# Performance work log

Hardware: AMD Instinct MI355X
Metric: run time of the kernel (lower is better)

## Reference

```python
import jax, jax.numpy as jnp
import numpy as np

R = 8      # num_dilation_rates
B = 32
C_IN = 21
C = 128    # C_out
L = 4096
K = 2      # kernel_size


def _causal_conv(x, w, dilation, pad, length):
    # x: [B, C, L], w: [Co, Ci, K]. Left-pad by `pad`, dilated valid conv, keep first L.
    # Matches Causal_conv1d: type 'A' -> pad=K(=2); type 'B' -> pad=dilation*(K-1)+1.
    y = jax.lax.conv_general_dilated(
        x, w, window_strides=(1,), padding=[(pad, 0)],
        rhs_dilation=(dilation,), dimension_numbers=('NCH', 'OIH', 'NCH'))
    return y[:, :, :length]


def setup_inputs() -> dict:
    key = jax.random.key(0)
    ks = jax.random.split(key, 10)
    s = 0.1  # small init scale (stands in for xavier)
    return {
        'x': jax.random.normal(ks[0], (B, C_IN, L), jnp.float32),
        'z': jax.random.normal(ks[1], (B, 1, L), jnp.float32),
        'w0': jax.random.normal(ks[2], (C, C_IN), jnp.float32) * s,          # causal_blocks[0] 1x1 conv
        'b0': jnp.zeros((C,), jnp.float32),
        'signal_w': jax.random.normal(ks[3], (R, C, C, K), jnp.float32) * s,  # dilated kernel-2 convs
        'gate_w': jax.random.normal(ks[4], (R, C, C, K), jnp.float32) * s,
        'cond_signal_w': jax.random.normal(ks[5], (R, C), jnp.float32) * s,   # Conv1d(1, C, 1) weights
        'cond_gate_w': jax.random.normal(ks[6], (R, C), jnp.float32) * s,
        'res_w': jax.random.normal(ks[7], (R, C, C), jnp.float32) * s,        # 1x1 residual convs
        'skip_w': jax.random.normal(ks[8], (R, C, C), jnp.float32) * s,       # 1x1 skip convs
    }


def reference(x, z, w0, b0, signal_w, gate_w, cond_signal_w, cond_gate_w, res_w, skip_w):
    length = x.shape[2]
    # initial 1x1 conv with bias
    h = jnp.einsum('oi,bil->bol', w0, x) + b0[None, :, None]
    orig = h
    cum_skip = jnp.zeros_like(h)
    zf = z[:, 0, :]  # [B, L]
    n_rates = signal_w.shape[0]
    for ii in range(n_rates):
        d = 2 ** ii
        pad = K if ii == 0 else d * (K - 1) + 1  # mask 'A' for layer 0, 'B' otherwise
        signal = _causal_conv(h, signal_w[ii], d, pad, length) \
            + jnp.einsum('o,bl->bol', cond_signal_w[ii], zf)
        gate = _causal_conv(h, gate_w[ii], d, pad, length) \
            + jnp.einsum('o,bl->bol', cond_gate_w[ii], zf)
        g = signal * jax.nn.sigmoid(gate)                      # gated activation
        skip = jnp.einsum('oi,bil->bol', skip_w[ii], g)
        res = jnp.einsum('oi,bil->bol', res_w[ii], g)
        h = (orig + res) if ii == 0 else (res + g)             # matches torch control flow
        cum_skip = cum_skip + skip
    return h, cum_skip
```

## Files before the change

### kernel.cpp

```cpp
#include <hip/hip_runtime.h>
#include <hip/hip_bf16.h>

#define RR 8
#define BB 32
#define CIN 21
#define CC 128
#define LL 4096
#define TT 64
#define SROW 132
#define GP 136
#define PADT 132
#define LP (LL + PADT)

typedef short s16x8 __attribute__((ext_vector_type(8)));
typedef float f32x4 __attribute__((ext_vector_type(4)));

__device__ __forceinline__ unsigned short f2b(float f) {
    __hip_bfloat16 h = __float2bfloat16(f);
    return *reinterpret_cast<unsigned short*>(&h);
}
__device__ __forceinline__ float b2f(unsigned short u) {
    __hip_bfloat16 h;
    *reinterpret_cast<unsigned short*>(&h) = u;
    return __bfloat162float(h);
}
__device__ __forceinline__ unsigned int packsplit(float v) {
    unsigned short hi = f2b(v);
    unsigned short lo = f2b(v - b2f(hi));
    return ((unsigned int)hi << 16) | (unsigned int)lo;
}
__device__ __forceinline__ float unpacksum(unsigned int u) {
    return b2f((unsigned short)(u >> 16)) + b2f((unsigned short)(u & 0xffffu));
}

__device__ __forceinline__ void unpack8(const unsigned int* p, s16x8& hi, s16x8& lo) {
    uint4 u0 = *reinterpret_cast<const uint4*>(p);
    uint4 u1 = *reinterpret_cast<const uint4*>(p + 4);
    union { int i[4]; s16x8 v; } H, L;
    H.i[0] = __builtin_amdgcn_perm(u0.y, u0.x, 0x07060302u);
    L.i[0] = __builtin_amdgcn_perm(u0.y, u0.x, 0x05040100u);
    H.i[1] = __builtin_amdgcn_perm(u0.w, u0.z, 0x07060302u);
    L.i[1] = __builtin_amdgcn_perm(u0.w, u0.z, 0x05040100u);
    H.i[2] = __builtin_amdgcn_perm(u1.y, u1.x, 0x07060302u);
    L.i[2] = __builtin_amdgcn_perm(u1.y, u1.x, 0x05040100u);
    H.i[3] = __builtin_amdgcn_perm(u1.w, u1.z, 0x07060302u);
    L.i[3] = __builtin_amdgcn_perm(u1.w, u1.z, 0x05040100u);
    hi = H.v; lo = L.v;
}

__global__ void prep_kernel(const float* __restrict__ sw, const float* __restrict__ gw,
                            const float* __restrict__ skw, const float* __restrict__ rew,
                            unsigned short* __restrict__ WsgH, unsigned short* __restrict__ WsgL,
                            unsigned short* __restrict__ WkrH, unsigned short* __restrict__ WkrL) {
    int idx = blockIdx.x * 256 + threadIdx.x;
    int r = idx >> 16;
    int rem = idx & 65535;
    int o = rem >> 8;
    int k = rem & 255;
    int c = k & 127;
    int tap = k >> 7;
    float v = (o < 128) ? sw[(((r * 128 + o) * 128 + c) << 1) + tap]
                        : gw[(((r * 128 + (o - 128)) * 128 + c) << 1) + tap];
    unsigned short hi = f2b(v);
    WsgH[idx] = hi;
    WsgL[idx] = f2b(v - b2f(hi));
    if (idx < RR * 256 * 128) {
        int r2 = idx >> 15;
        int rem2 = idx & 32767;
        int o2 = rem2 >> 7;
        int c2 = rem2 & 127;
        float v2 = (o2 < 128) ? skw[(r2 * 128 + o2) * 128 + c2]
                              : rew[(r2 * 128 + (o2 - 128)) * 128 + c2];
        unsigned short hi2 = f2b(v2);
        WkrH[idx] = hi2;
        WkrL[idx] = f2b(v2 - b2f(hi2));
    }
}

__global__ void zero_pad_kernel(unsigned int* __restrict__ hA, unsigned int* __restrict__ hB) {
    int idx = blockIdx.x * 256 + threadIdx.x;
    int c = idx & 127;
    int r = (idx >> 7) % PADT;
    int b = idx / (PADT * 128);
    size_t off = ((size_t)b * LP + r) * CC + c;
    hA[off] = 0u;
    hB[off] = 0u;
}

__global__ void proj_kernel(const float* __restrict__ x, const float* __restrict__ w0,
                            const float* __restrict__ b0, unsigned int* __restrict__ h0) {
    int idx = blockIdx.x * 256 + threadIdx.x;
    int c = idx & 127;
    int t = (idx >> 7) & (LL - 1);
    int b = idx >> 19;
    const float* xb = x + (size_t)b * CIN * LL + t;
    const float* w = w0 + c * CIN;
    float acc = b0[c];
#pragma unroll
    for (int i = 0; i < CIN; i++) acc = fmaf(w[i], xb[i * LL], acc);
    h0[((size_t)b * LP + PADT + t) * CC + c] = packsplit(acc);
}

__global__ void __launch_bounds__(512, 4) layer_kernel(
    const unsigned int* __restrict__ hcur,
    unsigned int* __restrict__ hnext,
    float* __restrict__ skipbuf,
    const unsigned short* __restrict__ WsgH, const unsigned short* __restrict__ WsgL,
    const unsigned short* __restrict__ WkrH, const unsigned short* __restrict__ WkrL,
    const float* __restrict__ csw, const float* __restrict__ cgw,
    const float* __restrict__ z,
    float* __restrict__ out,
    int off0, int first, int last) {
    __shared__ unsigned int sBuf[2 * TT * GP / 2];
    unsigned short* sGhi = (unsigned short*)sBuf;
    unsigned short* sGlo = sGhi + TT * GP;

    int tid = threadIdx.x;
    int b = blockIdx.x >> 6;
    int t0 = (blockIdx.x & 63) * TT;

    int wave = tid >> 6;
    int lane = tid & 63;
    int l15 = lane & 15;
    int quad = lane >> 4;

    const unsigned int* hb = hcur + (size_t)b * LP * CC;

    uint4 stg[4];
    {
        const unsigned int* src0 = hb + (size_t)(PADT + t0 - off0) * CC;
#pragma unroll
        for (int j = 0; j < 4; j++) {
            int flat = tid + 512 * j;
            int row = flat >> 5;
            int c16 = flat & 31;
            uint4 v = *(const uint4*)(src0 + (size_t)row * CC + c16 * 4);
            *(uint4*)(sBuf + row * SROW + c16 * 4) = v;
        }
        const unsigned int* src1 = hb + (size_t)(PADT + t0 - 1) * CC;
#pragma unroll
        for (int j = 0; j < 4; j++) {
            int flat = tid + 512 * j;
            int row = flat >> 5;
            int c16 = flat & 31;
            stg[j] = *(const uint4*)(src1 + (size_t)row * CC + c16 * 4);
        }
    }
    __syncthreads();

    f32x4 acc1[4][2];
#pragma unroll
    for (int m = 0; m < 4; m++)
#pragma unroll
        for (int n = 0; n < 2; n++) acc1[m][n] = (f32x4){0.f, 0.f, 0.f, 0.f};

#pragma unroll
    for (int kk = 0; kk < 4; kk++) {
        const int cb = kk * 32 + quad * 8;
        s16x8 Ah[4], Al[4];
#pragma unroll
        for (int m = 0; m < 4; m++)
            unpack8(sBuf + (m * 16 + l15) * SROW + cb, Ah[m], Al[m]);
#pragma unroll
        for (int n = 0; n < 2; n++) {
            int o = (wave + 8 * n) * 16 + l15;
            s16x8 Bh = *(const s16x8*)(WsgH + o * 256 + kk * 32 + quad * 8);
            s16x8 Bl = *(const s16x8*)(WsgL + o * 256 + kk * 32 + quad * 8);
#pragma unroll
            for (int m = 0; m < 4; m++) {
                acc1[m][n] = __builtin_amdgcn_mfma_f32_16x16x32_bf16(Ah[m], Bh, acc1[m][n], 0, 0, 0);
                acc1[m][n] = __builtin_amdgcn_mfma_f32_16x16x32_bf16(Al[m], Bh, acc1[m][n], 0, 0, 0);
                acc1[m][n] = __builtin_amdgcn_mfma_f32_16x16x32_bf16(Ah[m], Bl, acc1[m][n], 0, 0, 0);
            }
        }
    }
    __syncthreads();

#pragma unroll
    for (int j = 0; j < 4; j++) {
        int flat = tid + 512 * j;
        int row = flat >> 5;
        int c16 = flat & 31;
        *(uint4*)(sBuf + row * SROW + c16 * 4) = stg[j];
    }
    __syncthreads();

#pragma unroll
    for (int kk = 0; kk < 4; kk++) {
        const int cb = kk * 32 + quad * 8;
        s16x8 Ah[4], Al[4];
#pragma unroll
        for (int m = 0; m < 4; m++)
            unpack8(sBuf + (m * 16 + l15) * SROW + cb, Ah[m], Al[m]);
#pragma unroll
        for (int n = 0; n < 2; n++) {
            int o = (wave + 8 * n) * 16 + l15;
            s16x8 Bh = *(const s16x8*)(WsgH + o * 256 + (kk + 4) * 32 + quad * 8);
            s16x8 Bl = *(const s16x8*)(WsgL + o * 256 + (kk + 4) * 32 + quad * 8);
#pragma unroll
            for (int m = 0; m < 4; m++) {
                acc1[m][n] = __builtin_amdgcn_mfma_f32_16x16x32_bf16(Ah[m], Bh, acc1[m][n], 0, 0, 0);
                acc1[m][n] = __builtin_amdgcn_mfma_f32_16x16x32_bf16(Al[m], Bh, acc1[m][n], 0, 0, 0);
                acc1[m][n] = __builtin_amdgcn_mfma_f32_16x16x32_bf16(Ah[m], Bl, acc1[m][n], 0, 0, 0);
            }
        }
    }

    float g[4][4];
    {
        const float* zb = z + (size_t)b * LL + t0;
        float cs = csw[wave * 16 + l15];
        float cg = cgw[wave * 16 + l15];
#pragma unroll
        for (int m = 0; m < 4; m++)
#pragma unroll
            for (int reg = 0; reg < 4; reg++) {
                float zv = zb[m * 16 + quad * 4 + reg];
                float s = fmaf(cs, zv, acc1[m][0][reg]);
                float t = fmaf(cg, zv, acc1[m][1][reg]);
                g[m][reg] = s / (1.f + __expf(-t));
            }
    }
    __syncthreads();

    {
        int c = wave * 16 + l15;
#pragma unroll
        for (int m = 0; m < 4; m++)
#pragma unroll
            for (int reg = 0; reg < 4; reg++) {
                int tl = m * 16 + quad * 4 + reg;
                float gv = g[m][reg];
                unsigned short hi = f2b(gv);
                sGhi[tl * GP + c] = hi;
                sGlo[tl * GP + c] = f2b(gv - b2f(hi));
            }
    }
    __syncthreads();

    f32x4 acc2[4][2];
#pragma unroll
    for (int m = 0; m < 4; m++)
#pragma unroll
        for (int n = 0; n < 2; n++) acc2[m][n] = (f32x4){0.f, 0.f, 0.f, 0.f};

#pragma unroll
    for (int kk = 0; kk < 4; kk++) {
        s16x8 Ah[4], Al[4];
#pragma unroll
        for (int m = 0; m < 4; m++) {
            int off = (m * 16 + l15) * GP + kk * 32 + quad * 8;
            Ah[m] = *(const s16x8*)(sGhi + off);
            Al[m] = *(const s16x8*)(sGlo + off);
        }
#pragma unroll
        for (int n = 0; n < 2; n++) {
            int o2 = (wave + 8 * n) * 16 + l15;
            s16x8 Bh = *(const s16x8*)(WkrH + o2 * 128 + kk * 32 + quad * 8);
            s16x8 Bl = *(const s16x8*)(WkrL + o2 * 128 + kk * 32 + quad * 8);
#pragma unroll
            for (int m = 0; m < 4; m++) {
                acc2[m][n] = __builtin_amdgcn_mfma_f32_16x16x32_bf16(Ah[m], Bh, acc2[m][n], 0, 0, 0);
                acc2[m][n] = __builtin_amdgcn_mfma_f32_16x16x32_bf16(Al[m], Bh, acc2[m][n], 0, 0, 0);
                acc2[m][n] = __builtin_amdgcn_mfma_f32_16x16x32_bf16(Ah[m], Bl, acc2[m][n], 0, 0, 0);
            }
        }
    }

#pragma unroll
    for (int m = 0; m < 4; m++) {
        int c = wave * 16 + l15;
#pragma unroll
        for (int reg = 0; reg < 4; reg++) {
            int t = t0 + m * 16 + quad * 4 + reg;
            size_t hidx = ((size_t)b * LP + PADT + t) * CC + c;
            size_t sidx = ((size_t)b * LL + t) * CC + c;
            float skp = acc2[m][0][reg];
            float res = acc2[m][1][reg];
            float hv, sv;
            if (first) {
                hv = res + unpacksum(hcur[hidx]);
                sv = skp;
            } else {
                hv = res + g[m][reg];
                sv = skp + skipbuf[sidx];
            }
            if (last) {
                size_t oidx = ((size_t)b * CC + c) * LL + t;
                out[oidx] = hv;
                out[(size_t)BB * CC * LL + oidx] = sv;
            } else {
                hnext[hidx] = packsplit(hv);
                skipbuf[sidx] = sv;
            }
        }
    }
}

extern "C" void kernel_launch(void* const* d_in, const int* in_sizes, int n_in,
                              void* d_out, int out_size, void* d_ws, size_t ws_size,
                              hipStream_t stream) {
    const float* x = (const float*)d_in[0];
    const float* z = (const float*)d_in[1];
    const float* w0 = (const float*)d_in[2];
    const float* b0 = (const float*)d_in[3];
    const float* sw = (const float*)d_in[4];
    const float* gw = (const float*)d_in[5];
    const float* csw = (const float*)d_in[6];
    const float* cgw = (const float*)d_in[7];
    const float* rew = (const float*)d_in[8];
    const float* skw = (const float*)d_in[9];

    const size_t HSZ = (size_t)BB * LP * CC;
    const size_t NCL = (size_t)BB * CC * LL;
    unsigned int* hA = (unsigned int*)d_ws;
    unsigned int* hB = hA + HSZ;
    float* skipb = (float*)(hB + HSZ);
    unsigned short* WsgH = (unsigned short*)(skipb + NCL);
    unsigned short* WsgL = WsgH + (size_t)RR * 256 * 256;
    unsigned short* WkrH = WsgL + (size_t)RR * 256 * 256;
    unsigned short* WkrL = WkrH + (size_t)RR * 256 * 128;

    prep_kernel<<<RR * 256 * 256 / 256, 256, 0, stream>>>(sw, gw, skw, rew, WsgH, WsgL, WkrH, WkrL);
    zero_pad_kernel<<<BB * PADT * 128 / 256, 256, 0, stream>>>(hA, hB);
    proj_kernel<<<NCL / 256, 256, 0, stream>>>(x, w0, b0, hA);

    unsigned int* hc = hA;
    unsigned int* hn = hB;
    for (int ii = 0; ii < RR; ii++) {
        int d = 1 << ii;
        int off0 = d + 1;
        layer_kernel<<<BB * (LL / TT), 512, 0, stream>>>(
            hc, hn, skipb,
            WsgH + (size_t)ii * 256 * 256, WsgL + (size_t)ii * 256 * 256,
            WkrH + (size_t)ii * 256 * 128, WkrL + (size_t)ii * 256 * 128,
            csw + ii * CC, cgw + ii * CC, z,
            (float*)d_out, off0, ii == 0 ? 1 : 0, ii == RR - 1 ? 1 : 0);
        unsigned int* tmp = hc; hc = hn; hn = tmp;
    }
}
```

Baseline: 1.501 ms.

## Load both conv tap windows directly to LDS with XOR-swizzled layout

Replaces register-staged global loads and padded-row LDS stores with direct global-to-LDS loads covering both dilation taps at once. The layout uses an XOR swizzle on 16-byte units instead of row padding to avoid bank conflicts. This removes the staging registers, the second store pass and two barriers, and merges the two K-loops into one. In exchange, LDS use grows to 64KB per block, which may reduce occupancy below the launch-bounds target.

```diff
diff --git a/kernel.cpp b/kernel.cpp
--- a/kernel.cpp
+++ b/kernel.cpp
@@ -7,13 +7,14 @@
 #define CC 128
 #define LL 4096
 #define TT 64
-#define SROW 132
 #define GP 136
 #define PADT 132
 #define LP (LL + PADT)
 
 typedef short s16x8 __attribute__((ext_vector_type(8)));
 typedef float f32x4 __attribute__((ext_vector_type(4)));
+typedef unsigned int __attribute__((address_space(1))) gu32;
+typedef unsigned int __attribute__((address_space(3))) lu32;
 
 __device__ __forceinline__ unsigned short f2b(float f) {
     __hip_bfloat16 h = __float2bfloat16(f);
@@ -33,9 +34,7 @@
     return b2f((unsigned short)(u >> 16)) + b2f((unsigned short)(u & 0xffffu));
 }
 
-__device__ __forceinline__ void unpack8(const unsigned int* p, s16x8& hi, s16x8& lo) {
-    uint4 u0 = *reinterpret_cast<const uint4*>(p);
-    uint4 u1 = *reinterpret_cast<const uint4*>(p + 4);
+__device__ __forceinline__ void unpack2(uint4 u0, uint4 u1, s16x8& hi, s16x8& lo) {
     union { int i[4]; s16x8 v; } H, L;
     H.i[0] = __builtin_amdgcn_perm(u0.y, u0.x, 0x07060302u);
     L.i[0] = __builtin_amdgcn_perm(u0.y, u0.x, 0x05040100u);
@@ -111,7 +110,7 @@
     const float* __restrict__ z,
     float* __restrict__ out,
     int off0, int first, int last) {
-    __shared__ unsigned int sBuf[2 * TT * GP / 2];
+    __shared__ unsigned int sBuf[16384];
     unsigned short* sGhi = (unsigned short*)sBuf;
     unsigned short* sGlo = sGhi + TT * GP;
 
@@ -126,24 +125,18 @@
 
     const unsigned int* hb = hcur + (size_t)b * LP * CC;
 
-    uint4 stg[4];
     {
         const unsigned int* src0 = hb + (size_t)(PADT + t0 - off0) * CC;
-#pragma unroll
-        for (int j = 0; j < 4; j++) {
-            int flat = tid + 512 * j;
-            int row = flat >> 5;
-            int c16 = flat & 31;
-            uint4 v = *(const uint4*)(src0 + (size_t)row * CC + c16 * 4);
-            *(uint4*)(sBuf + row * SROW + c16 * 4) = v;
-        }
         const unsigned int* src1 = hb + (size_t)(PADT + t0 - 1) * CC;
 #pragma unroll
-        for (int j = 0; j < 4; j++) {
-            int flat = tid + 512 * j;
-            int row = flat >> 5;
-            int c16 = flat & 31;
-            stg[j] = *(const uint4*)(src1 + (size_t)row * CC + c16 * 4);
+        for (int jj = 0; jj < 8; jj++) {
+            int flat = tid + 512 * jj;
+            int row = (flat >> 5) & 63;
+            int ud = flat & 31;
+            const unsigned int* srcw = (jj < 4) ? src0 : src1;
+            const unsigned int* gp = srcw + (size_t)row * CC + ((ud ^ (row & 7)) << 2);
+            unsigned int* lp = sBuf + flat * 4;
+            __builtin_amdgcn_global_load_lds((const gu32*)gp, (lu32*)lp, 16, 0, 0);
         }
     }
     __syncthreads();
@@ -155,48 +148,24 @@
         for (int n = 0; n < 2; n++) acc1[m][n] = (f32x4){0.f, 0.f, 0.f, 0.f};
 
 #pragma unroll
-    for (int kk = 0; kk < 4; kk++) {
-        const int cb = kk * 32 + quad * 8;
+    for (int kk = 0; kk < 8; kk++) {
+        const int win = kk >> 2;
+        const int U = (kk & 3) * 8 + quad * 2;
         s16x8 Ah[4], Al[4];
 #pragma unroll
-        for (int m = 0; m < 4; m++)
-            unpack8(sBuf + (m * 16 + l15) * SROW + cb, Ah[m], Al[m]);
+        for (int m = 0; m < 4; m++) {
+            int r = m * 16 + l15;
+            const unsigned int* base = sBuf + win * 8192 + r * 128;
+            int s = r & 7;
+            uint4 x0 = *(const uint4*)(base + ((U ^ s) << 2));
+            uint4 x1 = *(const uint4*)(base + (((U + 1) ^ s) << 2));
+            unpack2(x0, x1, Ah[m], Al[m]);
+        }
 #pragma unroll
         for (int n = 0; n < 2; n++) {
             int o = (wave + 8 * n) * 16 + l15;
             s16x8 Bh = *(const s16x8*)(WsgH + o * 256 + kk * 32 + quad * 8);
             s16x8 Bl = *(const s16x8*)(WsgL + o * 256 + kk * 32 + quad * 8);
-#pragma unroll
-            for (int m = 0; m < 4; m++) {
-                acc1[m][n] = __builtin_amdgcn_mfma_f32_16x16x32_bf16(Ah[m], Bh, acc1[m][n], 0, 0, 0);
-                acc1[m][n] = __builtin_amdgcn_mfma_f32_16x16x32_bf16(Al[m], Bh, acc1[m][n], 0, 0, 0);
-                acc1[m][n] = __builtin_amdgcn_mfma_f32_16x16x32_bf16(Ah[m], Bl, acc1[m][n], 0, 0, 0);
-            }
-        }
-    }
-    __syncthreads();
-
-#pragma unroll
-    for (int j = 0; j < 4; j++) {
-        int flat = tid + 512 * j;
-        int row = flat >> 5;
-        int c16 = flat & 31;
-        *(uint4*)(sBuf + row * SROW + c16 * 4) = stg[j];
-    }
-    __syncthreads();
-
-#pragma unroll
-    for (int kk = 0; kk < 4; kk++) {
-        const int cb = kk * 32 + quad * 8;
-        s16x8 Ah[4], Al[4];
-#pragma unroll
-        for (int m = 0; m < 4; m++)
-            unpack8(sBuf + (m * 16 + l15) * SROW + cb, Ah[m], Al[m]);
-#pragma unroll
-        for (int n = 0; n < 2; n++) {
-            int o = (wave + 8 * n) * 16 + l15;
-            s16x8 Bh = *(const s16x8*)(WsgH + o * 256 + (kk + 4) * 32 + quad * 8);
-            s16x8 Bl = *(const s16x8*)(WsgL + o * 256 + (kk + 4) * 32 + quad * 8);
 #pragma unroll
             for (int m = 0; m < 4; m++) {
                 acc1[m][n] = __builtin_amdgcn_mfma_f32_16x16x32_bf16(Ah[m], Bh, acc1[m][n], 0, 0, 0);
```

Measured after the change: 1.322 ms. 1.13x faster.
